# Performance work log

Hardware: AMD Instinct MI355X
Metric: run time of the kernel (lower is better)

Reference implementation:

```python
import jax, jax.numpy as jnp
import numpy as np

ALPHA = 0.5


def setup_inputs() -> dict:
    key = jax.random.key(0)
    k1, k2 = jax.random.split(key)
    inputs = jax.random.normal(k1, (16384,), dtype=jnp.float32)
    targets = jax.random.normal(k2, (16384,), dtype=jnp.float32)
    return {"inputs": inputs, "targets": targets}


def reference(inputs, targets):
    # Chamfer 1D: mean over x of min_j |x_i - y_j|, symmetrized with weight alpha.
    x = inputs.reshape(-1)
    y = targets.reshape(-1)
    n = x.shape[0]
    m = y.shape[0]
    # Pairwise absolute differences [N, M]; min over each axis gives both directions.
    d = jnp.abs(x[:, None] - y[None, :])
    cd_xy = jnp.sum(jnp.min(d, axis=1))  # sum_i min_j |x_i - y_j|
    cd_yx = jnp.sum(jnp.min(d, axis=0))  # sum_j min_i |y_j - x_i|
    return ALPHA * cd_xy / n + (1.0 - ALPHA) * cd_yx / m
```

## Files before the change

kernel.cpp:

```cpp
#include <hip/hip_runtime.h>
#include <cfloat>

#define TPB 256
#define Q 8
#define CHUNKS 64
#define LTILE 2048
#define RBLK 128
#define ALPHA 0.5f

__device__ __forceinline__ float min3abs(float acc, float d0, float d1) {
    float r;
    asm("v_min3_f32 %0, %1, |%2|, |%3|"
        : "=v"(r) : "v"(acc), "v"(d0), "v"(d1));
    return r;
}

__device__ __forceinline__ void group_compute(const float4 a, const float4 b,
                                              const float qv[Q], float acc[Q]) {
#pragma unroll
    for (int k = 0; k < Q; ++k) {
        const float q = qv[k];
        float acc_k = acc[k];
        acc_k = min3abs(acc_k, a.x - q, a.y - q);
        acc_k = min3abs(acc_k, a.z - q, a.w - q);
        acc_k = min3abs(acc_k, b.x - q, b.y - q);
        acc_k = min3abs(acc_k, b.z - q, b.w - q);
        acc[k] = acc_k;
    }
}

__global__ __launch_bounds__(TPB) void
chamfer_scan(const float* __restrict__ x, const float* __restrict__ y,
             int n, int m, int nbx, float* __restrict__ partial) {
    __shared__ float s_db[LTILE] __attribute__((aligned(16)));

    const bool side_x = ((int)blockIdx.y < nbx);
    const float* __restrict__ qsrc = side_x ? x : y;
    const float* __restrict__ db   = side_x ? y : x;
    const int qn  = side_x ? n : m;
    const int dbn = side_x ? m : n;
    const int by  = side_x ? (int)blockIdx.y : (int)blockIdx.y - nbx;

    const int qoff = (by * TPB + (int)threadIdx.x) * Q;
    const int total = n + m;
    const int gbase = side_x ? qoff : n + qoff;
    const bool live = (qoff < qn);

    float qv[Q];
    if (live && qoff + Q <= qn) {
        const float4* __restrict__ q4 = (const float4*)(qsrc + qoff);
        const float4 qa = q4[0], qb = q4[1];
        qv[0] = qa.x; qv[1] = qa.y; qv[2] = qa.z; qv[3] = qa.w;
        qv[4] = qb.x; qv[5] = qb.y; qv[6] = qb.z; qv[7] = qb.w;
    } else {
#pragma unroll
        for (int k = 0; k < Q; ++k)
            qv[k] = live ? qsrc[min(qoff + k, qn - 1)] : 0.0f;
    }

    const int chunk_len = (dbn + CHUNKS - 1) / CHUNKS;
    const int start = (int)blockIdx.x * chunk_len;
    const int end = min(start + chunk_len, dbn);

    float acc[Q];
#pragma unroll
    for (int k = 0; k < Q; ++k) acc[k] = FLT_MAX;

    for (int ts = start; ts < end; ts += LTILE) {
        const int tlen = min(LTILE, end - ts);
        for (int i = threadIdx.x; i < tlen; i += TPB) s_db[i] = db[ts + i];
        __syncthreads();

        const float4* __restrict__ s4 = (const float4*)s_db;
        const int ng = tlen >> 3;
        if (ng > 0) {
            float4 a0 = s4[0], b0 = s4[1];
            int g = 0;
            for (; g + 1 < ng; ++g) {
                const float4 a1 = s4[2 * g + 2];
                const float4 b1 = s4[2 * g + 3];
                group_compute(a0, b0, qv, acc);
                a0 = a1; b0 = b1;
            }
            group_compute(a0, b0, qv, acc);
        }
        for (int j = ng << 3; j < tlen; ++j) {
            const float v = s_db[j];
#pragma unroll
            for (int k = 0; k < Q; ++k) acc[k] = fminf(acc[k], fabsf(qv[k] - v));
        }
        __syncthreads();
    }

    if (!live) return;
    float* __restrict__ dst = partial + (size_t)blockIdx.x * total + gbase;
    if (qoff + Q <= qn) {
#pragma unroll
        for (int k = 0; k < Q; ++k) dst[k] = acc[k];
    } else {
#pragma unroll
        for (int k = 0; k < Q; ++k)
            if (qoff + k < qn) dst[k] = acc[k];
    }
}

__global__ __launch_bounds__(TPB) void
chamfer_reduce1(const float* __restrict__ vals, int n, int m,
                double* __restrict__ bsums) {
    const int total = n + m;
    const int lq = threadIdx.x & (RBLK - 1);
    const int h = threadIdx.x >> 7;
    const int q = blockIdx.x * RBLK + lq;

    float mv = FLT_MAX;
    if (q < total) {
        const int c0 = h * (CHUNKS / 2), c1 = c0 + CHUNKS / 2;
        for (int c = c0; c < c1; ++c)
            mv = fminf(mv, vals[(size_t)c * total + q]);
    }
    __shared__ float half1[RBLK];
    if (h == 1) half1[lq] = mv;
    __syncthreads();

    double sx = 0.0, sy = 0.0;
    if (h == 0 && q < total) {
        const float best = fminf(mv, half1[lq]);
        if (q < n) sx = (double)best; else sy = (double)best;
    }
    for (int off = 32; off > 0; off >>= 1) {
        sx += __shfl_down(sx, off);
        sy += __shfl_down(sy, off);
    }
    __shared__ double wsx[2], wsy[2];
    if (h == 0 && (threadIdx.x & 63) == 0) {
        wsx[threadIdx.x >> 6] = sx;
        wsy[threadIdx.x >> 6] = sy;
    }
    __syncthreads();
    if (threadIdx.x == 0) {
        bsums[2 * blockIdx.x]     = wsx[0] + wsx[1];
        bsums[2 * blockIdx.x + 1] = wsy[0] + wsy[1];
    }
}

__global__ __launch_bounds__(TPB) void
chamfer_reduce2(const double* __restrict__ bsums, int nb,
                int n, int m, float* __restrict__ out) {
    double sx = 0.0, sy = 0.0;
    for (int i = threadIdx.x; i < nb; i += blockDim.x) {
        sx += bsums[2 * i];
        sy += bsums[2 * i + 1];
    }
    for (int off = 32; off > 0; off >>= 1) {
        sx += __shfl_down(sx, off);
        sy += __shfl_down(sy, off);
    }
    __shared__ double lsx[4], lsy[4];
    const int wave = threadIdx.x >> 6;
    if ((threadIdx.x & 63) == 0) { lsx[wave] = sx; lsy[wave] = sy; }
    __syncthreads();
    if (threadIdx.x == 0) {
        double tx = 0.0, ty = 0.0;
        for (int w = 0; w < (int)(blockDim.x >> 6); ++w) { tx += lsx[w]; ty += lsy[w]; }
        const double a = (double)ALPHA;
        out[0] = (float)(a * tx / (double)n + (1.0 - a) * ty / (double)m);
    }
}

extern "C" void kernel_launch(void* const* d_in, const int* in_sizes, int n_in,
                              void* d_out, int out_size, void* d_ws, size_t ws_size,
                              hipStream_t stream) {
    const float* x = (const float*)d_in[0];
    const float* y = (const float*)d_in[1];
    const int n = in_sizes[0];
    const int m = in_sizes[1];
    float* out = (float*)d_out;
    const int total = n + m;

    const int qpb = TPB * Q;
    const int nbx = (n + qpb - 1) / qpb;
    const int nby = (m + qpb - 1) / qpb;
    const dim3 grid1(CHUNKS, nbx + nby);
    const int nb1 = (total + RBLK - 1) / RBLK;

    const size_t partial_bytes = (size_t)CHUNKS * total * sizeof(float);
    const size_t partial_aligned = (partial_bytes + 255) & ~(size_t)255;

    float* partial = (float*)d_ws;
    double* bsums = (double*)((char*)d_ws + partial_aligned);

    chamfer_scan<<<grid1, TPB, 0, stream>>>(x, y, n, m, nbx, partial);
    chamfer_reduce1<<<nb1, TPB, 0, stream>>>(partial, n, m, bsums);
    chamfer_reduce2<<<1, TPB, 0, stream>>>(bsums, nb1, n, m, out);
}
```

Baseline: 80.31 us.

## Replace brute-force pairwise scan with bucketed nearest-neighbor search

Swaps the O(N*M) all-pairs min-abs-difference scan for a bucket sort approach. Each element is histogrammed into fixed-range buckets, prefix scans give bucket offsets, and running max/min give the nearest neighbors in adjacent nonempty buckets. Elements are then scattered into sorted buckets, and each query checks its own bucket plus those neighbor extremes. The bucket range [-8,8) is fixed, which suits the normal-distributed inputs. Values outside the range are clamped into the edge buckets, which keeps the result correct but can slow things down. The change adds several small launches, a memset, and atomics in place of the heavy compute.

```diff
diff --git a/kernel.cpp b/kernel.cpp
--- a/kernel.cpp
+++ b/kernel.cpp
@@ -2,150 +2,185 @@
 #include <cfloat>
 
 #define TPB 256
-#define Q 8
-#define CHUNKS 64
-#define LTILE 2048
-#define RBLK 128
+#define SCANT 1024
+#define BKT 32768
+#define EPT (BKT / SCANT)
+#define RLO -8.0f
+#define RSCALE (BKT / 16.0f)
 #define ALPHA 0.5f
 
-__device__ __forceinline__ float min3abs(float acc, float d0, float d1) {
-    float r;
-    asm("v_min3_f32 %0, %1, |%2|, |%3|"
-        : "=v"(r) : "v"(acc), "v"(d0), "v"(d1));
+__device__ __forceinline__ unsigned enc_f(float v) {
+    unsigned u = __float_as_uint(v);
+    return (u & 0x80000000u) ? ~u : (u | 0x80000000u);
+}
+__device__ __forceinline__ float dec_f(unsigned e) {
+    unsigned u = (e & 0x80000000u) ? (e & 0x7FFFFFFFu) : ~e;
+    return __uint_as_float(u);
+}
+__device__ __forceinline__ int bucket_of(float v) {
+    int b = (int)((v - RLO) * RSCALE);
+    return min(max(b, 0), BKT - 1);
+}
+
+
+__global__ __launch_bounds__(TPB) void
+chamfer_hist(const float* __restrict__ x, const float* __restrict__ y,
+             int n, int m, unsigned* __restrict__ ws) {
+    const int i = blockIdx.x * TPB + threadIdx.x;
+    if (i >= n + m) return;
+    const bool isx = i < n;
+    const float v = isx ? x[i] : y[i - n];
+    const int side = isx ? 0 : 1;
+    const int b = bucket_of(v);
+    const unsigned e = enc_f(v);
+    atomicAdd(ws + 0 * BKT + side * BKT + b, 1u);
+    atomicMax(ws + 2 * BKT + side * BKT + b, e);
+    atomicMax(ws + 4 * BKT + side * BKT + b, ~e);
+}
+
+template <int OP>
+__device__ __forceinline__ unsigned opf(unsigned a, unsigned b) {
+    return OP == 0 ? (a + b) : (a > b ? a : b);
+}
+
+template <int OP>
+__device__ unsigned blk_excl_scan(unsigned agg, unsigned* stmp) {
+    const int lane = threadIdx.x & 63;
+    const int w = threadIdx.x >> 6;
+    unsigned incl = agg;
+#pragma unroll
+    for (int off = 1; off < 64; off <<= 1) {
+        const unsigned u = __shfl_up(incl, off);
+        if (lane >= off) incl = opf<OP>(incl, u);
+    }
+    unsigned ex = __shfl_up(incl, 1);
+    if (lane == 0) ex = 0u;
+    if (lane == 63) stmp[w] = incl;
+    __syncthreads();
+    if (threadIdx.x == 0) {
+        unsigned run = 0u;
+#pragma unroll
+        for (int i = 0; i < SCANT / 64; ++i) {
+            const unsigned v = stmp[i];
+            stmp[i] = run;
+            run = opf<OP>(run, v);
+        }
+    }
+    __syncthreads();
+    const unsigned r = opf<OP>(stmp[w], ex);
+    __syncthreads();
     return r;
 }
 
-__device__ __forceinline__ void group_compute(const float4 a, const float4 b,
-                                              const float qv[Q], float acc[Q]) {
-#pragma unroll
-    for (int k = 0; k < Q; ++k) {
-        const float q = qv[k];
-        float acc_k = acc[k];
-        acc_k = min3abs(acc_k, a.x - q, a.y - q);
-        acc_k = min3abs(acc_k, a.z - q, a.w - q);
-        acc_k = min3abs(acc_k, b.x - q, b.y - q);
-        acc_k = min3abs(acc_k, b.z - q, b.w - q);
-        acc[k] = acc_k;
-    }
-}
-
-__global__ __launch_bounds__(TPB) void
-chamfer_scan(const float* __restrict__ x, const float* __restrict__ y,
-             int n, int m, int nbx, float* __restrict__ partial) {
-    __shared__ float s_db[LTILE] __attribute__((aligned(16)));
-
-    const bool side_x = ((int)blockIdx.y < nbx);
-    const float* __restrict__ qsrc = side_x ? x : y;
-    const float* __restrict__ db   = side_x ? y : x;
-    const int qn  = side_x ? n : m;
-    const int dbn = side_x ? m : n;
-    const int by  = side_x ? (int)blockIdx.y : (int)blockIdx.y - nbx;
-
-    const int qoff = (by * TPB + (int)threadIdx.x) * Q;
+__global__ __launch_bounds__(SCANT) void chamfer_scans(unsigned* __restrict__ ws) {
+    __shared__ unsigned stmp[SCANT / 64];
+    const int t = threadIdx.x;
+#pragma unroll
+    for (int side = 0; side < 2; ++side) {
+        {
+            unsigned* cnt = ws + 0 * BKT + side * BKT;
+            unsigned* start = ws + 6 * BKT + side * BKT;
+            unsigned* work = ws + 8 * BKT + side * BKT;
+            const int base = t * EPT;
+            unsigned c[EPT], agg = 0;
+#pragma unroll
+            for (int i = 0; i < EPT; ++i) { c[i] = cnt[base + i]; agg += c[i]; }
+            unsigned run = blk_excl_scan<0>(agg, stmp);
+#pragma unroll
+            for (int i = 0; i < EPT; ++i) {
+                start[base + i] = run;
+                work[base + i] = run;
+                run += c[i];
+            }
+        }
+        {
+            unsigned* A = ws + 2 * BKT + side * BKT;
+            const int base = t * EPT;
+            unsigned a[EPT], agg = 0;
+#pragma unroll
+            for (int i = 0; i < EPT; ++i) { a[i] = A[base + i]; agg = opf<1>(agg, a[i]); }
+            unsigned run = blk_excl_scan<1>(agg, stmp);
+#pragma unroll
+            for (int i = 0; i < EPT; ++i) { run = opf<1>(run, a[i]); A[base + i] = run; }
+        }
+        {
+            unsigned* A = ws + 4 * BKT + side * BKT;
+            const int base = (SCANT - 1 - t) * EPT;
+            unsigned a[EPT], agg = 0;
+#pragma unroll
+            for (int i = 0; i < EPT; ++i) { a[i] = A[base + i]; agg = opf<1>(agg, a[i]); }
+            unsigned run = blk_excl_scan<1>(agg, stmp);
+#pragma unroll
+            for (int i = EPT - 1; i >= 0; --i) { run = opf<1>(run, a[i]); A[base + i] = run; }
+        }
+    }
+}
+
+__global__ __launch_bounds__(TPB) void
+chamfer_scatter(const float* __restrict__ x, const float* __restrict__ y,
+                int n, int m, unsigned* __restrict__ ws) {
+    const int i = blockIdx.x * TPB + threadIdx.x;
+    if (i >= n + m) return;
+    const bool isx = i < n;
+    const float v = isx ? x[i] : y[i - n];
+    const int side = isx ? 0 : 1;
+    const int b = bucket_of(v);
+    const unsigned pos = atomicAdd(ws + 8 * BKT + side * BKT + b, 1u);
+    float* sorted = (float*)(ws + 10 * BKT) + (isx ? 0 : n);
+    sorted[pos] = v;
+}
+
+__global__ __launch_bounds__(TPB) void
+chamfer_query(const float* __restrict__ x, const float* __restrict__ y,
+              int n, int m, const unsigned* __restrict__ ws,
+              double* __restrict__ bsums) {
+    const int q = blockIdx.x * TPB + threadIdx.x;
     const int total = n + m;
-    const int gbase = side_x ? qoff : n + qoff;
-    const bool live = (qoff < qn);
-
-    float qv[Q];
-    if (live && qoff + Q <= qn) {
-        const float4* __restrict__ q4 = (const float4*)(qsrc + qoff);
-        const float4 qa = q4[0], qb = q4[1];
-        qv[0] = qa.x; qv[1] = qa.y; qv[2] = qa.z; qv[3] = qa.w;
-        qv[4] = qb.x; qv[5] = qb.y; qv[6] = qb.z; qv[7] = qb.w;
-    } else {
-#pragma unroll
-        for (int k = 0; k < Q; ++k)
-            qv[k] = live ? qsrc[min(qoff + k, qn - 1)] : 0.0f;
-    }
-
-    const int chunk_len = (dbn + CHUNKS - 1) / CHUNKS;
-    const int start = (int)blockIdx.x * chunk_len;
-    const int end = min(start + chunk_len, dbn);
-
-    float acc[Q];
-#pragma unroll
-    for (int k = 0; k < Q; ++k) acc[k] = FLT_MAX;
-
-    for (int ts = start; ts < end; ts += LTILE) {
-        const int tlen = min(LTILE, end - ts);
-        for (int i = threadIdx.x; i < tlen; i += TPB) s_db[i] = db[ts + i];
-        __syncthreads();
-
-        const float4* __restrict__ s4 = (const float4*)s_db;
-        const int ng = tlen >> 3;
-        if (ng > 0) {
-            float4 a0 = s4[0], b0 = s4[1];
-            int g = 0;
-            for (; g + 1 < ng; ++g) {
-                const float4 a1 = s4[2 * g + 2];
-                const float4 b1 = s4[2 * g + 3];
-                group_compute(a0, b0, qv, acc);
-                a0 = a1; b0 = b1;
-            }
-            group_compute(a0, b0, qv, acc);
-        }
-        for (int j = ng << 3; j < tlen; ++j) {
-            const float v = s_db[j];
-#pragma unroll
-            for (int k = 0; k < Q; ++k) acc[k] = fminf(acc[k], fabsf(qv[k] - v));
-        }
-        __syncthreads();
-    }
-
-    if (!live) return;
-    float* __restrict__ dst = partial + (size_t)blockIdx.x * total + gbase;
-    if (qoff + Q <= qn) {
-#pragma unroll
-        for (int k = 0; k < Q; ++k) dst[k] = acc[k];
-    } else {
-#pragma unroll
-        for (int k = 0; k < Q; ++k)
-            if (qoff + k < qn) dst[k] = acc[k];
-    }
-}
-
-__global__ __launch_bounds__(TPB) void
-chamfer_reduce1(const float* __restrict__ vals, int n, int m,
-                double* __restrict__ bsums) {
-    const int total = n + m;
-    const int lq = threadIdx.x & (RBLK - 1);
-    const int h = threadIdx.x >> 7;
-    const int q = blockIdx.x * RBLK + lq;
-
-    float mv = FLT_MAX;
+    double sx = 0.0, sy = 0.0;
     if (q < total) {
-        const int c0 = h * (CHUNKS / 2), c1 = c0 + CHUNKS / 2;
-        for (int c = c0; c < c1; ++c)
-            mv = fminf(mv, vals[(size_t)c * total + q]);
-    }
-    __shared__ float half1[RBLK];
-    if (h == 1) half1[lq] = mv;
-    __syncthreads();
-
-    double sx = 0.0, sy = 0.0;
-    if (h == 0 && q < total) {
-        const float best = fminf(mv, half1[lq]);
-        if (q < n) sx = (double)best; else sy = (double)best;
+        const bool isx = q < n;
+        const float v = isx ? x[q] : y[q - n];
+        const int side = isx ? 1 : 0;
+        const unsigned* start = ws + 6 * BKT + side * BKT;
+        const unsigned* endw  = ws + 8 * BKT + side * BKT;
+        const unsigned* L     = ws + 2 * BKT + side * BKT;
+        const unsigned* Rc    = ws + 4 * BKT + side * BKT;
+        const float* sorted = (const float*)(ws + 10 * BKT) + (side ? n : 0);
+        const int b = bucket_of(v);
+        float best = FLT_MAX;
+        const unsigned s0 = start[b], e0 = endw[b];
+        for (unsigned i = s0; i < e0; ++i)
+            best = fminf(best, fabsf(v - sorted[i]));
+        if (b > 0) {
+            const unsigned le = L[b - 1];
+            if (le) best = fminf(best, fabsf(v - dec_f(le)));
+        }
+        if (b < BKT - 1) {
+            const unsigned ce = Rc[b + 1];
+            if (ce) best = fminf(best, fabsf(v - dec_f(~ce)));
+        }
+        if (isx) sx = (double)best; else sy = (double)best;
     }
     for (int off = 32; off > 0; off >>= 1) {
         sx += __shfl_down(sx, off);
         sy += __shfl_down(sy, off);
     }
-    __shared__ double wsx[2], wsy[2];
-    if (h == 0 && (threadIdx.x & 63) == 0) {
-        wsx[threadIdx.x >> 6] = sx;
-        wsy[threadIdx.x >> 6] = sy;
-    }
+    __shared__ double wsx[TPB / 64], wsy[TPB / 64];
+    const int w = threadIdx.x >> 6;
+    if ((threadIdx.x & 63) == 0) { wsx[w] = sx; wsy[w] = sy; }
     __syncthreads();
     if (threadIdx.x == 0) {
-        bsums[2 * blockIdx.x]     = wsx[0] + wsx[1];
-        bsums[2 * blockIdx.x + 1] = wsy[0] + wsy[1];
-    }
-}
-
-__global__ __launch_bounds__(TPB) void
-chamfer_reduce2(const double* __restrict__ bsums, int nb,
-                int n, int m, float* __restrict__ out) {
+        double tx = 0.0, ty = 0.0;
+#pragma unroll
+        for (int i = 0; i < TPB / 64; ++i) { tx += wsx[i]; ty += wsy[i]; }
+        bsums[2 * blockIdx.x] = tx;
+        bsums[2 * blockIdx.x + 1] = ty;
+    }
+}
+
+__global__ __launch_bounds__(TPB) void
+chamfer_final(const double* __restrict__ bsums, int nb,
+              int n, int m, float* __restrict__ out) {
     double sx = 0.0, sy = 0.0;
     for (int i = threadIdx.x; i < nb; i += blockDim.x) {
         sx += bsums[2 * i];
@@ -177,19 +212,17 @@
     float* out = (float*)d_out;
     const int total = n + m;
 
-    const int qpb = TPB * Q;
-    const int nbx = (n + qpb - 1) / qpb;
-    const int nby = (m + qpb - 1) / qpb;
-    const dim3 grid1(CHUNKS, nbx + nby);
-    const int nb1 = (total + RBLK - 1) / RBLK;
-
-    const size_t partial_bytes = (size_t)CHUNKS * total * sizeof(float);
-    const size_t partial_aligned = (partial_bytes + 255) & ~(size_t)255;
-
-    float* partial = (float*)d_ws;
-    double* bsums = (double*)((char*)d_ws + partial_aligned);
-
-    chamfer_scan<<<grid1, TPB, 0, stream>>>(x, y, n, m, nbx, partial);
-    chamfer_reduce1<<<nb1, TPB, 0, stream>>>(partial, n, m, bsums);
-    chamfer_reduce2<<<1, TPB, 0, stream>>>(bsums, nb1, n, m, out);
-}
+    unsigned* ws = (unsigned*)d_ws;
+    const size_t meta_bytes = ((size_t)10 * BKT + (size_t)total) * sizeof(unsigned);
+    const size_t meta_al = (meta_bytes + 255) & ~(size_t)255;
+    double* bsums = (double*)((char*)d_ws + meta_al);
+
+    const int nb = (total + TPB - 1) / TPB;
+
+    hipMemsetAsync(ws, 0, (size_t)6 * BKT * sizeof(unsigned), stream);
+    chamfer_hist<<<nb, TPB, 0, stream>>>(x, y, n, m, ws);
+    chamfer_scans<<<1, SCANT, 0, stream>>>(ws);
+    chamfer_scatter<<<nb, TPB, 0, stream>>>(x, y, n, m, ws);
+    chamfer_query<<<nb, TPB, 0, stream>>>(x, y, n, m, ws, bsums);
+    chamfer_final<<<1, TPB, 0, stream>>>(bsums, nb, n, m, out);
+}
```

New measurement: 136.1 us. 69.5% more time.
